# Kernel optimization log

Hardware: AMD Instinct MI355X
Metric: run time of the kernel (lower is better)

The kernel has to match this reference:

```python
import jax, jax.numpy as jnp
import numpy as np


def gcn_conv(x, edge_index, edge_weight, W, b):
    """PyG GCNConv: add self-loops (weight 1), symmetric degree norm, aggregate, linear."""
    N = x.shape[0]
    loop = jnp.arange(N, dtype=edge_index.dtype)
    src = jnp.concatenate([edge_index[0], loop])
    dst = jnp.concatenate([edge_index[1], loop])
    ew = jnp.concatenate([edge_weight, jnp.ones((N,), dtype=x.dtype)])
    deg = jax.ops.segment_sum(ew, dst, num_segments=N)
    dinv = jnp.where(deg > 0, jax.lax.rsqrt(deg), 0.0)
    norm = dinv[src] * ew * dinv[dst]            # [E+N]
    h = x @ W                                    # [N, out] transform first
    msg = h[src] * norm[:, None]                 # gather + scale
    out = jax.ops.segment_sum(msg, dst, num_segments=N)  # scatter-add
    return out + b


def l2norm(x, eps=1e-12):
    n = jnp.sqrt(jnp.sum(x * x, axis=-1, keepdims=True))
    return x / jnp.maximum(n, eps)


def setup_inputs() -> dict:
    key = jax.random.key(0)
    ks = jax.random.split(key, 16)
    N_net, E_net, N_dag, E_dag = 100000, 600000, 50000, 400000
    D_net, D_dag, H_net, H_dag = 128, 128, 128, 128
    s = lambda fan_in: 1.0 / np.sqrt(fan_in)
    return {
        "net_feat": jax.random.normal(ks[0], (N_net, D_net), jnp.float32),
        "net_edge_index": jax.random.randint(ks[1], (2, E_net), 0, N_net, jnp.int32),
        "net_edge_weights": jax.random.uniform(ks[2], (E_net,), jnp.float32),
        "dag_feat": jax.random.normal(ks[3], (N_dag, D_dag), jnp.float32),
        "dag_edge_index": jax.random.randint(ks[4], (2, E_dag), 0, N_dag, jnp.int32),
        "dag_edge_weights": jax.random.uniform(ks[5], (E_dag,), jnp.float32),
        "W_net": jax.random.normal(ks[6], (D_net, H_net), jnp.float32) * s(D_net),
        "b_net": jnp.zeros((H_net,), jnp.float32),
        "W_dag": jax.random.normal(ks[7], (D_dag, H_dag), jnp.float32) * s(D_dag),
        "b_dag": jnp.zeros((H_dag,), jnp.float32),
        "W1": jax.random.normal(ks[8], (H_net + H_dag, 64), jnp.float32) * s(H_net + H_dag),
        "b1": jnp.zeros((64,), jnp.float32),
        "W2": jax.random.normal(ks[9], (64, 1), jnp.float32) * s(64),
        "b2": jnp.zeros((1,), jnp.float32),
    }


def reference(net_feat, net_edge_index, net_edge_weights,
              dag_feat, dag_edge_index, dag_edge_weights,
              W_net, b_net, W_dag, b_dag, W1, b1, W2, b2):
    net_emb = jax.nn.relu(gcn_conv(net_feat, net_edge_index, net_edge_weights, W_net, b_net))
    dag_emb = jax.nn.relu(gcn_conv(dag_feat, dag_edge_index, dag_edge_weights, W_dag, b_dag))
    # normalize == True
    net_emb = l2norm(net_emb)
    dag_emb = l2norm(dag_emb)
    # net_batch/dag_batch are None: mean over nodes -> single state value
    net_vec = net_emb.mean(axis=0)
    dag_vec = dag_emb.mean(axis=0)
    combined = jnp.concatenate([net_vec, dag_vec], axis=-1)
    h = jax.nn.relu(combined @ W1 + b1)
    state_val = h @ W2 + b2
    return state_val
```

## Files before the change

kernel.cpp:

```cpp
#include <hip/hip_runtime.h>

#define FD 128
#define PAD 48
#define WSCALE 16777216.0f
#define WINV   5.9604645e-8f

typedef __attribute__((ext_vector_type(8))) short short8;
typedef __attribute__((ext_vector_type(4))) float f32x4;

__device__ inline unsigned short f2bf(float f) {
    unsigned u = __float_as_uint(f);
    return (unsigned short)((u + 0x7fffu + ((u >> 16) & 1u)) >> 16);
}
__device__ inline void bf4_to_f32(uint2 u, float& a, float& b, float& c, float& d) {
    a = __uint_as_float(u.x << 16);
    b = __uint_as_float(u.x & 0xffff0000u);
    c = __uint_as_float(u.y << 16);
    d = __uint_as_float(u.y & 0xffff0000u);
}
__device__ inline float pc_to_dinv(unsigned long long pv) {
    return rsqrtf((float)(pv & 0xffffffffull) * WINV + 1.0f);
}
__device__ inline void split1(float x, unsigned short& h, unsigned short& l) {
    unsigned u = __float_as_uint(x);
    unsigned hh = (u + 0x7fffu + ((u >> 16) & 1u)) >> 16;
    float r = x - __uint_as_float(hh << 16);
    unsigned u2 = __float_as_uint(r);
    h = (unsigned short)hh;
    l = (unsigned short)((u2 + 0x7fffu + ((u2 >> 16) & 1u)) >> 16);
}

__global__ __launch_bounds__(256) void bucket_pack(
        const int* __restrict__ ei_n, const float* __restrict__ ew_n,
        unsigned long long* __restrict__ pc_n, int2* __restrict__ el_n,
        int E_n, int GBn,
        const int* __restrict__ ei_d, const float* __restrict__ ew_d,
        unsigned long long* __restrict__ pc_d, int2* __restrict__ el_d,
        int E_d,
        const float* __restrict__ Wn, const float* __restrict__ Wd,
        unsigned short* __restrict__ Wpack) {
    int b = blockIdx.x;
    int packStart = (int)gridDim.x - 16;
    if (b >= packStart) {
        int p = b - packStart;
        int graph = p >> 3, pb = p & 7;
        const float* W = graph ? Wd : Wn;
        int c  = threadIdx.x & 127;
        int hh = threadIdx.x >> 7;
        int k0 = pb * 16 + hh * 8;
        short8 hv, lv;
        #pragma unroll
        for (int j = 0; j < 8; j++) {
            unsigned short hq, lq;
            split1(W[(k0 + j) * FD + c], hq, lq);
            hv[j] = (short)hq; lv[j] = (short)lq;
        }
        char* dst = (char*)Wpack + graph * 65536
                  + c * 256 + 16 * ((k0 >> 3) ^ (c & 15));
        *(short8*)dst = hv;
        *(short8*)(dst + 32768) = lv;
        return;
    }
    const int* ei; const float* ew; unsigned long long* pc; int2* el; int E, e;
    if (b < GBn) { ei = ei_n; ew = ew_n; pc = pc_n; el = el_n; E = E_n;
                   e = b * 256 + threadIdx.x; }
    else         { ei = ei_d; ew = ew_d; pc = pc_d; el = el_d; E = E_d;
                   e = (b - GBn) * 256 + threadIdx.x; }
    if (e < E) {
        int src = ei[e];
        int dst = ei[E + e];
        float w = ew[e];
        unsigned long long val =
            (1ull << 32) |
            (unsigned long long)(unsigned int)__float2uint_rn(w * WSCALE);
        unsigned long long old = atomicAdd(&pc[dst], val);
        unsigned int pos = (unsigned int)(old >> 32);
        if (pos < PAD)
            el[(size_t)dst * PAD + pos] = make_int2(src, __float_as_int(w));
    }
}

__global__ __launch_bounds__(256) void gemm_mfma(
        const float* __restrict__ X_n, const unsigned long long* __restrict__ pc_n,
        unsigned short* __restrict__ hs_n, int N_n, int Gn,
        const float* __restrict__ X_d, const unsigned long long* __restrict__ pc_d,
        unsigned short* __restrict__ hs_d, int N_d,
        const unsigned short* __restrict__ Wpack) {
    __shared__ unsigned short WL[2][128][128];

    const float* X; const unsigned long long* pc; unsigned short* hs; int N, r0;
    const char* wsrc;
    if (blockIdx.x < Gn) { X = X_n; pc = pc_n; hs = hs_n; N = N_n;
                           r0 = blockIdx.x * 128; wsrc = (const char*)Wpack; }
    else                 { X = X_d; pc = pc_d; hs = hs_d; N = N_d;
                           r0 = (blockIdx.x - Gn) * 128;
                           wsrc = (const char*)Wpack + 65536; }

    const int tid  = threadIdx.x;
    const int w    = tid >> 6;
    const int lane = tid & 63;
    const int c15  = lane & 15;
    const int g    = lane >> 4;

    {
        const float4* s4 = (const float4*)wsrc;
        float4* d4 = (float4*)WL;
        #pragma unroll
        for (int i = 0; i < 16; i++) d4[tid + i * 256] = s4[tid + i * 256];
    }
    __syncthreads();

    f32x4 acc[2][8] = {};

    const int row0 = r0 + 32 * w + c15;
    const float* x0p = X + (size_t)row0 * FD;
    const float* x1p = x0p + 16 * FD;
    const bool v0 = row0 < N, v1 = (row0 + 16) < N;

    #pragma unroll
    for (int kt = 0; kt < 4; kt++) {
        const int ko = 32 * kt + 8 * g;
        float4 a0 = {}, a1 = {}, c0 = {}, c1 = {};
        if (v0) { a0 = *(const float4*)(x0p + ko); c0 = *(const float4*)(x0p + ko + 4); }
        if (v1) { a1 = *(const float4*)(x1p + ko); c1 = *(const float4*)(x1p + ko + 4); }
        short8 ah0, al0, ah1, al1;
        {
            float xx[8] = {a0.x, a0.y, a0.z, a0.w, c0.x, c0.y, c0.z, c0.w};
            #pragma unroll
            for (int j = 0; j < 8; j++) {
                unsigned short hq, lq; split1(xx[j], hq, lq);
                ah0[j] = (short)hq; al0[j] = (short)lq;
            }
        }
        {
            float xx[8] = {a1.x, a1.y, a1.z, a1.w, c1.x, c1.y, c1.z, c1.w};
            #pragma unroll
            for (int j = 0; j < 8; j++) {
                unsigned short hq, lq; split1(xx[j], hq, lq);
                ah1[j] = (short)hq; al1[j] = (short)lq;
            }
        }

        const char* bbase = (const char*)WL + c15 * 256
                          + 16 * (((unsigned)(g + 4 * kt)) ^ (unsigned)c15);
        #pragma unroll
        for (int cf = 0; cf < 8; cf++) {
            short8 bh = *(const short8*)(bbase + cf * 4096);
            short8 bl = *(const short8*)(bbase + cf * 4096 + 32768);
            acc[0][cf] = __builtin_amdgcn_mfma_f32_16x16x32_bf16(ah0, bh, acc[0][cf], 0, 0, 0);
            acc[1][cf] = __builtin_amdgcn_mfma_f32_16x16x32_bf16(ah1, bh, acc[1][cf], 0, 0, 0);
            acc[0][cf] = __builtin_amdgcn_mfma_f32_16x16x32_bf16(al0, bh, acc[0][cf], 0, 0, 0);
            acc[1][cf] = __builtin_amdgcn_mfma_f32_16x16x32_bf16(al1, bh, acc[1][cf], 0, 0, 0);
            acc[0][cf] = __builtin_amdgcn_mfma_f32_16x16x32_bf16(ah0, bl, acc[0][cf], 0, 0, 0);
            acc[1][cf] = __builtin_amdgcn_mfma_f32_16x16x32_bf16(ah1, bl, acc[1][cf], 0, 0, 0);
        }
    }

    __syncthreads();
    unsigned short* OT = (unsigned short*)WL;
    #pragma unroll
    for (int rf = 0; rf < 2; rf++) {
        float dv[4];
        #pragma unroll
        for (int r = 0; r < 4; r++) {
            int row = r0 + 32 * w + 16 * rf + 4 * g + r;
            dv[r] = pc_to_dinv(row < N ? pc[row] : 0ull);
        }
        #pragma unroll
        for (int cf = 0; cf < 8; cf++) {
            #pragma unroll
            for (int r = 0; r < 4; r++) {
                int lrow = 32 * w + 16 * rf + 4 * g + r;
                unsigned byteo = (unsigned)(lrow * 256)
                               + (unsigned)((32 * cf + 2 * c15) ^ ((lrow & 15) << 4));
                *(unsigned short*)((char*)OT + byteo) = f2bf(acc[rf][cf][r] * dv[r]);
            }
        }
    }
    __syncthreads();
    #pragma unroll
    for (int p = 0; p < 8; p++) {
        int idx  = p * 256 + tid;
        int lrow = idx >> 4, ch = idx & 15;
        int row  = r0 + lrow;
        if (row < N) {
            uint4 v = *(const uint4*)((const char*)WL + lrow * 256
                                      + 16 * (ch ^ (lrow & 15)));
            *(uint4*)&hs[(size_t)row * FD + ch * 8] = v;
        }
    }
}

__global__ __launch_bounds__(256) void gather_reduce_both(
        const unsigned short* __restrict__ hs_n,
        const unsigned long long* __restrict__ pc_n, const int2* __restrict__ el_n,
        const float* __restrict__ b_n, int N_n,
        const unsigned short* __restrict__ hs_d,
        const unsigned long long* __restrict__ pc_d, const int2* __restrict__ el_d,
        const float* __restrict__ b_d, int N_d,
        float* __restrict__ vec) {
    __shared__ float accw[8][2 * FD];
    const int tid  = threadIdx.x;
    const int hw   = tid >> 5;
    const int sl   = tid & 31;

    float4 bbn = *(const float4*)&b_n[sl * 4];
    float4 bbd = *(const float4*)&b_d[sl * 4];
    float an0 = 0.f, an1 = 0.f, an2 = 0.f, an3 = 0.f;
    float ad0 = 0.f, ad1 = 0.f, ad2 = 0.f, ad3 = 0.f;

    const int total = N_n + N_d;
    const int S     = gridDim.x * 8;

    struct GMeta {
        unsigned long long pv;
        int2 my;
        uint2 self;
        const unsigned short* hs;
        const int2* el;
        int i;
    };

    auto loadMeta = [&](int t, GMeta& m) {
        const bool isn = t < N_n;
        const int i = isn ? t : t - N_n;
        m.i  = i;
        m.hs = isn ? hs_n : hs_d;
        m.el = (isn ? el_n : el_d) + (size_t)i * PAD;
        m.pv = (isn ? pc_n : pc_d)[i];
        m.my = (sl < 16) ? m.el[sl] : make_int2(0, 0);
        m.self = *(const uint2*)(m.hs + i * FD + sl * 4);
    };

    auto issueE = [&](const GMeta& m, uint2 (&e)[12]) {
        int cn = (int)(m.pv >> 32); if (cn > PAD) cn = PAD;
        #pragma unroll
        for (int u = 0; u < 12; u++) {
            int q  = __shfl(m.my.x, u, 32);
            int qq = (u < cn) ? q : m.i;
            e[u] = *(const uint2*)(m.hs + qq * FD + sl * 4);
        }
    };

    auto PHASE = [&](GMeta& mc, GMeta& mn, uint2 (&ec)[12], uint2 (&en)[12],
                     int t) {
        const bool isn = t < N_n;
        int cnt = (int)(mc.pv >> 32); if (cnt > PAD) cnt = PAD;
        const float dv = pc_to_dinv(mc.pv);
        const int2 mysv = mc.my;
        const unsigned short* hs_c = mc.hs;
        const int2* el_c = mc.el;
        const int  i_c  = mc.i;
        float s0, s1, s2, s3; bf4_to_f32(mc.self, s0, s1, s2, s3);
        float x0 = s0 * dv, x1 = s1 * dv, x2 = s2 * dv, x3 = s3 * dv;

        { int t2 = t + 2 * S; loadMeta(t2 < total ? t2 : 0, mc); }

        issueE(mn, en);

        #pragma unroll
        for (int u = 0; u < 12; u++) {
            int wi = __shfl(mysv.y, u, 32);
            float w = (u < cnt) ? __int_as_float(wi) * dv : 0.f;
            float a, b2, c, d; bf4_to_f32(ec[u], a, b2, c, d);
            x0 = fmaf(a, w, x0); x1 = fmaf(b2, w, x1);
            x2 = fmaf(c, w, x2); x3 = fmaf(d, w, x3);
        }
        if (cnt > 12) {
            uint2 et[4]; float wt[4];
            #pragma unroll
            for (int u = 0; u < 4; u++) {
                int jj = 12 + u;
                int q  = __shfl(mysv.x, jj, 32);
                int wi = __shfl(mysv.y, jj, 32);
                bool act = jj < cnt;
                wt[u] = act ? __int_as_float(wi) * dv : 0.f;
                int qq = act ? q : i_c;
                et[u] = *(const uint2*)(hs_c + qq * FD + sl * 4);
            }
            #pragma unroll
            for (int u = 0; u < 4; u++) {
                float a, b2, c, d; bf4_to_f32(et[u], a, b2, c, d);
                x0 = fmaf(a, wt[u], x0); x1 = fmaf(b2, wt[u], x1);
                x2 = fmaf(c, wt[u], x2); x3 = fmaf(d, wt[u], x3);
            }
            for (int j = 16; j < cnt; j++) {
                int2 p = el_c[j];
                float w = __int_as_float(p.y) * dv;
                uint2 u = *(const uint2*)(hs_c + p.x * FD + sl * 4);
                float a, b2, c, d; bf4_to_f32(u, a, b2, c, d);
                x0 = fmaf(a, w, x0); x1 = fmaf(b2, w, x1);
                x2 = fmaf(c, w, x2); x3 = fmaf(d, w, x3);
            }
        }

        float4 bb = isn ? bbn : bbd;
        x0 = fmaxf(x0 + bb.x, 0.f);
        x1 = fmaxf(x1 + bb.y, 0.f);
        x2 = fmaxf(x2 + bb.z, 0.f);
        x3 = fmaxf(x3 + bb.w, 0.f);
        float ss = fmaf(x0, x0, fmaf(x1, x1, fmaf(x2, x2, x3 * x3)));
        #pragma unroll
        for (int o = 16; o; o >>= 1) ss += __shfl_xor(ss, o);
        float inv = 1.0f / fmaxf(sqrtf(ss), 1e-12f);
        if (isn) {
            an0 = fmaf(x0, inv, an0); an1 = fmaf(x1, inv, an1);
            an2 = fmaf(x2, inv, an2); an3 = fmaf(x3, inv, an3);
        } else {
            ad0 = fmaf(x0, inv, ad0); ad1 = fmaf(x1, inv, ad1);
            ad2 = fmaf(x2, inv, ad2); ad3 = fmaf(x3, inv, ad3);
        }
    };

    int t = blockIdx.x * 8 + hw;
    if (t < total) {
        GMeta mA, mB;
        uint2 e1[12], e2[12];
        loadMeta(t, mA);
        { int ts = t + S; loadMeta(ts < total ? ts : 0, mB); }
        issueE(mA, e1);
        while (true) {
            PHASE(mA, mB, e1, e2, t);
            t += S; if (t >= total) break;
            PHASE(mB, mA, e2, e1, t);
            t += S; if (t >= total) break;
        }
    }

    accw[hw][sl * 4 + 0] = an0;
    accw[hw][sl * 4 + 1] = an1;
    accw[hw][sl * 4 + 2] = an2;
    accw[hw][sl * 4 + 3] = an3;
    accw[hw][FD + sl * 4 + 0] = ad0;
    accw[hw][FD + sl * 4 + 1] = ad1;
    accw[hw][FD + sl * 4 + 2] = ad2;
    accw[hw][FD + sl * 4 + 3] = ad3;
    __syncthreads();
    {
        float s = accw[0][tid] + accw[1][tid] + accw[2][tid] + accw[3][tid]
                + accw[4][tid] + accw[5][tid] + accw[6][tid] + accw[7][tid];
        unsafeAtomicAdd(&vec[tid], s);
    }
}

__global__ __launch_bounds__(256) void final_kernel(
        const float* __restrict__ vec,
        const float* __restrict__ W1, const float* __restrict__ b1,
        const float* __restrict__ W2, const float* __restrict__ b2,
        float* __restrict__ out, float invNnet, float invNdag) {
    __shared__ float part[4][64];
    int j = threadIdx.x & 63;
    int q = threadIdx.x >> 6;
    float h = 0.f;
    for (int k = q * 64; k < q * 64 + 64; k++) {
        float sc = (k < 128) ? invNnet : invNdag;
        h = fmaf(vec[k] * sc, W1[k * 64 + j], h);
    }
    part[q][j] = h;
    __syncthreads();
    if (threadIdx.x < 64) {
        float hh = b1[j] + part[0][j] + part[1][j] + part[2][j] + part[3][j];
        hh = fmaxf(hh, 0.f);
        float p = hh * W2[j];
        #pragma unroll
        for (int o = 32; o; o >>= 1) p += __shfl_xor(p, o);
        if (j == 0) out[0] = p + b2[0];
    }
}

extern "C" void kernel_launch(void* const* d_in, const int* in_sizes, int n_in,
                              void* d_out, int out_size, void* d_ws, size_t ws_size,
                              hipStream_t stream) {
    const float* net_feat = (const float*)d_in[0];
    const int*   net_ei   = (const int*)d_in[1];
    const float* net_ew   = (const float*)d_in[2];
    const float* dag_feat = (const float*)d_in[3];
    const int*   dag_ei   = (const int*)d_in[4];
    const float* dag_ew   = (const float*)d_in[5];
    const float* W_net    = (const float*)d_in[6];
    const float* b_net    = (const float*)d_in[7];
    const float* W_dag    = (const float*)d_in[8];
    const float* b_dag    = (const float*)d_in[9];
    const float* W1       = (const float*)d_in[10];
    const float* b1       = (const float*)d_in[11];
    const float* W2       = (const float*)d_in[12];
    const float* b2       = (const float*)d_in[13];

    const int N_net = in_sizes[0] / FD;
    const int E_net = in_sizes[2];
    const int N_dag = in_sizes[3] / FD;
    const int E_dag = in_sizes[5];
    const int GBn = (E_net + 255) / 256, GBd = (E_dag + 255) / 256;
    const int Gn  = (N_net + 127) / 128, Gd  = (N_dag + 127) / 128;

    char* w = (char*)d_ws;
    size_t o = 0;
    unsigned short* hs_net = (unsigned short*)(w + o); o += (size_t)2 * N_net * FD;
    unsigned short* hs_dag = (unsigned short*)(w + o); o += (size_t)2 * N_dag * FD;
    unsigned long long* pc_net = (unsigned long long*)(w + o); o += (size_t)8 * N_net;
    unsigned long long* pc_dag = (unsigned long long*)(w + o); o += (size_t)8 * N_dag;
    float* vec = (float*)(w + o); o += 256 * 4;
    size_t zbytes = (size_t)8 * (N_net + N_dag) + 256 * 4;
    int2* elist_net = (int2*)(w + o); o += (size_t)8 * N_net * PAD;
    int2* elist_dag = (int2*)(w + o); o += (size_t)8 * N_dag * PAD;
    unsigned short* Wpack = (unsigned short*)(w + o); o += 131072;

    hipMemsetAsync(pc_net, 0, zbytes, stream);

    bucket_pack<<<GBn + GBd + 16, 256, 0, stream>>>(
        net_ei, net_ew, pc_net, elist_net, E_net, GBn,
        dag_ei, dag_ew, pc_dag, elist_dag, E_dag,
        W_net, W_dag, Wpack);

    gemm_mfma<<<Gn + Gd, 256, 0, stream>>>(
        net_feat, pc_net, hs_net, N_net, Gn,
        dag_feat, pc_dag, hs_dag, N_dag, Wpack);

    gather_reduce_both<<<2048, 256, 0, stream>>>(
        hs_net, pc_net, elist_net, b_net, N_net,
        hs_dag, pc_dag, elist_dag, b_dag, N_dag, vec);

    final_kernel<<<1, 256, 0, stream>>>(vec, W1, b1, W2, b2, (float*)d_out,
                                        1.0f / (float)N_net, 1.0f / (float)N_dag);
}
```

Baseline: 338.6 us.

## Stage gathered neighbor rows through LDS via async global_load_lds ring buffer

The gather-reduce kernel now prefetches the 12 neighbor feature rows per node with global_load_lds into a per-wave double-buffered LDS ring instead of holding them in registers. It uses an explicit vmcnt wait to overlap the next node's loads with the current node's accumulation. The grid shrinks from 2048 to 768 blocks with a fixed iteration count, and the feature-slice mapping changes to fit the 4-byte LDS load layout. This is meant to cut register pressure and deepen memory-level parallelism. The cost is a hand-tuned waitcnt that must stay exactly in step with the issued loads, plus more LDS use.

Result: faster. 316.9 us (-6.4%).

```diff
diff --git a/kernel.cpp b/kernel.cpp
--- a/kernel.cpp
+++ b/kernel.cpp
@@ -4,6 +4,7 @@
 #define PAD 48
 #define WSCALE 16777216.0f
 #define WINV   5.9604645e-8f
+#define GGRID 768
 
 typedef __attribute__((ext_vector_type(8))) short short8;
 typedef __attribute__((ext_vector_type(4))) float f32x4;
@@ -28,6 +29,11 @@
     unsigned u2 = __float_as_uint(r);
     h = (unsigned short)hh;
     l = (unsigned short)((u2 + 0x7fffu + ((u2 >> 16) & 1u)) >> 16);
+}
+__device__ __forceinline__ void gl_lds4(const void* g, void* l) {
+    __builtin_amdgcn_global_load_lds(
+        (const __attribute__((address_space(1))) unsigned int*)g,
+        (__attribute__((address_space(3))) unsigned int*)l, 4, 0, 0);
 }
 
 __global__ __launch_bounds__(256) void bucket_pack(
@@ -199,102 +205,105 @@
         const unsigned long long* __restrict__ pc_d, const int2* __restrict__ el_d,
         const float* __restrict__ b_d, int N_d,
         float* __restrict__ vec) {
-    __shared__ float accw[8][2 * FD];
+    __shared__ char ring[4][2][12][512];
+
     const int tid  = threadIdx.x;
+    const int wv   = tid >> 6;
+    const int lane = tid & 63;
+    const int h    = lane >> 5;
+    const int sl   = lane & 31;
     const int hw   = tid >> 5;
-    const int sl   = tid & 31;
-
-    float4 bbn = *(const float4*)&b_n[sl * 4];
-    float4 bbd = *(const float4*)&b_d[sl * 4];
+
+    const int loff = (sl < 16) ? (h * 128 + sl * 8) : (256 + h * 128 + (sl - 16) * 8);
+    const int fo   = (sl < 16) ? (sl * 4) : (64 + (sl - 16) * 4);
+
+    float4 bbn = *(const float4*)&b_n[fo];
+    float4 bbd = *(const float4*)&b_d[fo];
     float an0 = 0.f, an1 = 0.f, an2 = 0.f, an3 = 0.f;
     float ad0 = 0.f, ad1 = 0.f, ad2 = 0.f, ad3 = 0.f;
 
     const int total = N_n + N_d;
-    const int S     = gridDim.x * 8;
-
-    struct GMeta {
+    const int S     = GGRID * 8;
+    const int t0    = blockIdx.x * 8 + hw;
+    const int tA0   = blockIdx.x * 8 + 2 * wv;
+    const int nIter = (total - tA0 + S - 1) / S;
+
+    struct Meta {
         unsigned long long pv;
         int2 my;
         uint2 self;
         const unsigned short* hs;
         const int2* el;
-        int i;
+        int i, isn, valid;
     };
 
-    auto loadMeta = [&](int t, GMeta& m) {
-        const bool isn = t < N_n;
-        const int i = isn ? t : t - N_n;
+    auto loadMeta = [&](int t) {
+        Meta m;
+        m.valid = (t < total);
+        int tt = m.valid ? t : 0;
+        m.isn = (tt < N_n);
+        int i = m.isn ? tt : tt - N_n;
         m.i  = i;
-        m.hs = isn ? hs_n : hs_d;
-        m.el = (isn ? el_n : el_d) + (size_t)i * PAD;
-        m.pv = (isn ? pc_n : pc_d)[i];
+        m.hs = m.isn ? hs_n : hs_d;
+        m.el = (m.isn ? el_n : el_d) + (size_t)i * PAD;
+        m.pv = (m.isn ? pc_n : pc_d)[i];
         m.my = (sl < 16) ? m.el[sl] : make_int2(0, 0);
-        m.self = *(const uint2*)(m.hs + i * FD + sl * 4);
+        m.self = *(const uint2*)(m.hs + (size_t)i * FD + fo);
+        return m;
     };
 
-    auto issueE = [&](const GMeta& m, uint2 (&e)[12]) {
+    auto issueEdges = [&](const Meta& m, char* buf) {
         int cn = (int)(m.pv >> 32); if (cn > PAD) cn = PAD;
+        const char* base = (const char*)m.hs;
         #pragma unroll
         for (int u = 0; u < 12; u++) {
             int q  = __shfl(m.my.x, u, 32);
             int qq = (u < cn) ? q : m.i;
-            e[u] = *(const uint2*)(m.hs + qq * FD + sl * 4);
+            const char* g = base + (size_t)qq * 256 + sl * 4;
+            gl_lds4(g,       buf + u * 512);
+            gl_lds4(g + 128, buf + u * 512 + 256);
         }
     };
 
-    auto PHASE = [&](GMeta& mc, GMeta& mn, uint2 (&ec)[12], uint2 (&en)[12],
-                     int t) {
-        const bool isn = t < N_n;
-        int cnt = (int)(mc.pv >> 32); if (cnt > PAD) cnt = PAD;
-        const float dv = pc_to_dinv(mc.pv);
-        const int2 mysv = mc.my;
-        const unsigned short* hs_c = mc.hs;
-        const int2* el_c = mc.el;
-        const int  i_c  = mc.i;
-        float s0, s1, s2, s3; bf4_to_f32(mc.self, s0, s1, s2, s3);
+    auto consume = [&](const Meta& m, const char* buf) {
+        int cnt = (int)(m.pv >> 32); if (cnt > PAD) cnt = PAD;
+        const float dv = pc_to_dinv(m.pv);
+        float s0, s1, s2, s3; bf4_to_f32(m.self, s0, s1, s2, s3);
         float x0 = s0 * dv, x1 = s1 * dv, x2 = s2 * dv, x3 = s3 * dv;
-
-        { int t2 = t + 2 * S; loadMeta(t2 < total ? t2 : 0, mc); }
-
-        issueE(mn, en);
-
         #pragma unroll
         for (int u = 0; u < 12; u++) {
-            int wi = __shfl(mysv.y, u, 32);
+            uint2 e = *(const uint2*)(buf + u * 512 + loff);
+            int wi = __shfl(m.my.y, u, 32);
             float w = (u < cnt) ? __int_as_float(wi) * dv : 0.f;
-            float a, b2, c, d; bf4_to_f32(ec[u], a, b2, c, d);
+            float a, b2, c, d; bf4_to_f32(e, a, b2, c, d);
             x0 = fmaf(a, w, x0); x1 = fmaf(b2, w, x1);
             x2 = fmaf(c, w, x2); x3 = fmaf(d, w, x3);
         }
-        if (cnt > 12) {
-            uint2 et[4]; float wt[4];
+        if (__any(cnt > 12)) {
             #pragma unroll
-            for (int u = 0; u < 4; u++) {
-                int jj = 12 + u;
-                int q  = __shfl(mysv.x, jj, 32);
-                int wi = __shfl(mysv.y, jj, 32);
-                bool act = jj < cnt;
-                wt[u] = act ? __int_as_float(wi) * dv : 0.f;
-                int qq = act ? q : i_c;
-                et[u] = *(const uint2*)(hs_c + qq * FD + sl * 4);
-            }
-            #pragma unroll
-            for (int u = 0; u < 4; u++) {
-                float a, b2, c, d; bf4_to_f32(et[u], a, b2, c, d);
-                x0 = fmaf(a, wt[u], x0); x1 = fmaf(b2, wt[u], x1);
-                x2 = fmaf(c, wt[u], x2); x3 = fmaf(d, wt[u], x3);
-            }
-            for (int j = 16; j < cnt; j++) {
-                int2 p = el_c[j];
-                float w = __int_as_float(p.y) * dv;
-                uint2 u = *(const uint2*)(hs_c + p.x * FD + sl * 4);
-                float a, b2, c, d; bf4_to_f32(u, a, b2, c, d);
+            for (int u = 12; u < 16; u++) {
+                int q  = __shfl(m.my.x, u, 32);
+                int wi = __shfl(m.my.y, u, 32);
+                bool act = (u < cnt);
+                float w = act ? __int_as_float(wi) * dv : 0.f;
+                int qq = act ? q : m.i;
+                uint2 e = *(const uint2*)((const char*)m.hs + (size_t)qq * 256 + fo * 2);
+                float a, b2, c, d; bf4_to_f32(e, a, b2, c, d);
                 x0 = fmaf(a, w, x0); x1 = fmaf(b2, w, x1);
                 x2 = fmaf(c, w, x2); x3 = fmaf(d, w, x3);
             }
-        }
-
-        float4 bb = isn ? bbn : bbd;
+            if (__any(cnt > 16)) {
+                for (int j = 16; j < cnt; j++) {
+                    int2 p = m.el[j];
+                    float w = __int_as_float(p.y) * dv;
+                    uint2 e = *(const uint2*)((const char*)m.hs + (size_t)p.x * 256 + fo * 2);
+                    float a, b2, c, d; bf4_to_f32(e, a, b2, c, d);
+                    x0 = fmaf(a, w, x0); x1 = fmaf(b2, w, x1);
+                    x2 = fmaf(c, w, x2); x3 = fmaf(d, w, x3);
+                }
+            }
+        }
+        float4 bb = m.isn ? bbn : bbd;
         x0 = fmaxf(x0 + bb.x, 0.f);
         x1 = fmaxf(x1 + bb.y, 0.f);
         x2 = fmaxf(x2 + bb.z, 0.f);
@@ -303,7 +312,8 @@
         #pragma unroll
         for (int o = 16; o; o >>= 1) ss += __shfl_xor(ss, o);
         float inv = 1.0f / fmaxf(sqrtf(ss), 1e-12f);
-        if (isn) {
+        inv = m.valid ? inv : 0.f;
+        if (m.isn) {
             an0 = fmaf(x0, inv, an0); an1 = fmaf(x1, inv, an1);
             an2 = fmaf(x2, inv, an2); an3 = fmaf(x3, inv, an3);
         } else {
@@ -312,33 +322,40 @@
         }
     };
 
-    int t = blockIdx.x * 8 + hw;
-    if (t < total) {
-        GMeta mA, mB;
-        uint2 e1[12], e2[12];
-        loadMeta(t, mA);
-        { int ts = t + S; loadMeta(ts < total ? ts : 0, mB); }
-        issueE(mA, e1);
-        while (true) {
-            PHASE(mA, mB, e1, e2, t);
-            t += S; if (t >= total) break;
-            PHASE(mB, mA, e2, e1, t);
-            t += S; if (t >= total) break;
-        }
-    }
-
-    accw[hw][sl * 4 + 0] = an0;
-    accw[hw][sl * 4 + 1] = an1;
-    accw[hw][sl * 4 + 2] = an2;
-    accw[hw][sl * 4 + 3] = an3;
-    accw[hw][FD + sl * 4 + 0] = ad0;
-    accw[hw][FD + sl * 4 + 1] = ad1;
-    accw[hw][FD + sl * 4 + 2] = ad2;
-    accw[hw][FD + sl * 4 + 3] = ad3;
+    char* cur = &ring[wv][0][0][0];
+    char* nxt = &ring[wv][1][0][0];
+
+    Meta m0 = loadMeta(t0);
+    Meta m1 = loadMeta(t0 + S);
+    issueEdges(m0, cur);
+
+    for (int it = 0; it < nIter; ++it) {
+        Meta m2 = loadMeta(t0 + (it + 2) * S);
+        issueEdges(m1, nxt);
+        asm volatile("s_waitcnt vmcnt(27)" ::: "memory");
+        __builtin_amdgcn_sched_barrier(0);
+        consume(m0, cur);
+        m0 = m1; m1 = m2;
+        char* tmp = cur; cur = nxt; nxt = tmp;
+    }
+
+    asm volatile("s_waitcnt vmcnt(0)" ::: "memory");
+    __syncthreads();
+    float* accw = (float*)ring;
+    accw[hw * 256 + fo + 0] = an0;
+    accw[hw * 256 + fo + 1] = an1;
+    accw[hw * 256 + fo + 2] = an2;
+    accw[hw * 256 + fo + 3] = an3;
+    accw[hw * 256 + 128 + fo + 0] = ad0;
+    accw[hw * 256 + 128 + fo + 1] = ad1;
+    accw[hw * 256 + 128 + fo + 2] = ad2;
+    accw[hw * 256 + 128 + fo + 3] = ad3;
     __syncthreads();
     {
-        float s = accw[0][tid] + accw[1][tid] + accw[2][tid] + accw[3][tid]
-                + accw[4][tid] + accw[5][tid] + accw[6][tid] + accw[7][tid];
+        float s = accw[0 * 256 + tid] + accw[1 * 256 + tid]
+                + accw[2 * 256 + tid] + accw[3 * 256 + tid]
+                + accw[4 * 256 + tid] + accw[5 * 256 + tid]
+                + accw[6 * 256 + tid] + accw[7 * 256 + tid];
         unsafeAtomicAdd(&vec[tid], s);
     }
 }
@@ -416,7 +433,7 @@
         net_feat, pc_net, hs_net, N_net, Gn,
         dag_feat, pc_dag, hs_dag, N_dag, Wpack);
 
-    gather_reduce_both<<<2048, 256, 0, stream>>>(
+    gather_reduce_both<<<GGRID, 256, 0, stream>>>(
         hs_net, pc_net, elist_net, b_net, N_net,
         hs_dag, pc_dag, elist_dag, b_dag, N_dag, vec);
 
```
